# Optimization experiments

Measured on AMD Instinct MI355X. Metric: run time of the kernel, lower is better.

Reference implementation:

```python
import jax, jax.numpy as jnp
import numpy as np

N = 100000      # nodes
E = 1600000     # edges (before self-loops)
IN = 256        # input features
HID = 128       # hidden channels
HEADS = 8
C = HID // HEADS  # per-head channels = 16
L = 3           # num GAT layers
EPS = 1e-5      # batchnorm eps
NEG_SLOPE = 0.2 # leaky relu slope (PyG GATConv default)


def setup_inputs() -> dict:
    key = jax.random.key(0)
    ks = jax.random.split(key, 8)
    s = 0.05
    x = jax.random.normal(ks[0], (N, IN), jnp.float32)
    edge_index = jax.random.randint(ks[1], (2, E), 0, N, dtype=jnp.int32)
    proj_w = jax.random.normal(ks[2], (IN, HID), jnp.float32) * s
    proj_b = jnp.zeros((HID,), jnp.float32)
    W = jax.random.normal(ks[3], (L, HID, HID), jnp.float32) * s
    att_src = jax.random.normal(ks[4], (L, HEADS, C), jnp.float32) * s
    att_dst = jax.random.normal(ks[5], (L, HEADS, C), jnp.float32) * s
    conv_b = jnp.zeros((L, HID), jnp.float32)
    bn_g = jnp.ones((L, HID), jnp.float32)
    bn_b = jnp.zeros((L, HID), jnp.float32)
    fc_w = jax.random.normal(ks[6], (HID, 1), jnp.float32) * s
    fc_b = jnp.zeros((1,), jnp.float32)
    return {"x": x, "edge_index": edge_index, "proj_w": proj_w, "proj_b": proj_b,
            "W": W, "att_src": att_src, "att_dst": att_dst, "conv_b": conv_b,
            "bn_g": bn_g, "bn_b": bn_b, "fc_w": fc_w, "fc_b": fc_b}


def _gat_layer(x, src, dst, W, a_src, a_dst, b):
    # x: [N, HID] -> per-head features h: [N, HEADS, C]
    h = (x @ W).reshape(N, HEADS, C)
    al_src = jnp.einsum('nhc,hc->nh', h, a_src)  # [N, HEADS]
    al_dst = jnp.einsum('nhc,hc->nh', h, a_dst)  # [N, HEADS]
    e = jax.nn.leaky_relu(al_src[src] + al_dst[dst], NEG_SLOPE)  # [Etot, HEADS]
    # segment softmax over edges grouped by destination node
    m = jax.ops.segment_max(e, dst, num_segments=N)              # [N, HEADS]
    w = jnp.exp(e - m[dst])
    denom = jax.ops.segment_sum(w, dst, num_segments=N)          # [N, HEADS]
    alpha = w / (denom[dst] + 1e-16)                             # [Etot, HEADS]
    msg = h[src] * alpha[:, :, None]                             # [Etot, HEADS, C]
    out = jax.ops.segment_sum(msg, dst, num_segments=N)          # [N, HEADS, C]
    return out.reshape(N, HID) + b


def reference(x, edge_index, proj_w, proj_b, W, att_src, att_dst, conv_b, bn_g, bn_b, fc_w, fc_b):
    # add self loops (PyG GATConv default)
    loops = jnp.arange(N, dtype=edge_index.dtype)
    src = jnp.concatenate([edge_index[0], loops])
    dst = jnp.concatenate([edge_index[1], loops])
    h = jax.nn.elu(x @ proj_w + proj_b)
    for i in range(L):
        res = h
        h = _gat_layer(h, src, dst, W[i], att_src[i], att_dst[i], conv_b[i])
        mu = h.mean(axis=0)
        var = h.var(axis=0)  # biased, matches torch BN training math
        h = (h - mu) / jnp.sqrt(var + EPS) * bn_g[i] + bn_b[i]
        h = jax.nn.elu(h)
        h = h + res  # residual; dropout is identity in eval mode
    return h @ fc_w + fc_b
```

## Files before the change

kernel.cpp:

```cpp
#include <hip/hip_runtime.h>
#include <hip/hip_bf16.h>

#define NN 100000
#define EE 1600000
#define ETOT (NN + EE)
#define HID 128
#define HEADS 8
#define CH 16
#define EPS_BN 1e-5f
#define NEG_SLOPE 0.2f
#define NB 196
#define NBLK_A 208

typedef unsigned short ushort_t;
typedef unsigned int uint_t;
typedef __attribute__((ext_vector_type(8))) short short8;
typedef __attribute__((ext_vector_type(4))) float float4v;

__device__ inline uint_t f2bf(float x) {
    __hip_bfloat16 b = __float2bfloat16(x);
    return (uint_t)*reinterpret_cast<unsigned short*>(&b);
}
__device__ inline uint_t pack2(float lo, float hi) {
    return f2bf(lo) | (f2bf(hi) << 16);
}
__device__ inline float bf_lo(uint_t u) { return __uint_as_float(u << 16); }
__device__ inline float bf_hi(uint_t u) { return __uint_as_float(u & 0xffff0000u); }

__global__ __launch_bounds__(256) void bucket_hist(const int* __restrict__ ei,
                                                   int* bcnt, int* lbase) {
    __shared__ int h[256];
    int t = threadIdx.x;
    h[t] = 0;
    __syncthreads();
    int base = blockIdx.x * 8192;
    #pragma unroll 4
    for (int j = 0; j < 32; ++j) {
        int i = base + j * 256 + t;
        if (i < ETOT) {
            int d = (i < EE) ? ei[EE + i] : (i - EE);
            atomicAdd(&h[d >> 9], 1);
        }
    }
    __syncthreads();
    if (t < NB) {
        int v = h[t];
        lbase[blockIdx.x * NB + t] = v ? atomicAdd(&bcnt[t], v) : 0;
    }
}

__global__ void bucket_scan(const int* __restrict__ bcnt, int* bbase, int* rowptr) {
    __shared__ int s[256];
    int t = threadIdx.x;
    int orig = (t < NB) ? bcnt[t] : 0;
    s[t] = orig;
    __syncthreads();
    for (int off = 1; off < 256; off <<= 1) {
        int add = (t >= off) ? s[t - off] : 0;
        __syncthreads();
        s[t] += add;
        __syncthreads();
    }
    if (t < NB) bbase[t] = s[t] - orig;
    if (t == 0) { bbase[NB] = ETOT; rowptr[NN] = ETOT; }
}

__global__ __launch_bounds__(256) void bucket_scatter(const int* __restrict__ ei,
                                                      const int* __restrict__ bbase,
                                                      const int* __restrict__ lbase,
                                                      uint_t* __restrict__ pairs) {
    __shared__ int sbase[256];
    __shared__ int h[256];
    int t = threadIdx.x;
    sbase[t] = (t < NB) ? (bbase[t] + lbase[blockIdx.x * NB + t]) : 0;
    h[t] = 0;
    __syncthreads();
    int base = blockIdx.x * 8192;
    #pragma unroll 4
    for (int j = 0; j < 32; ++j) {
        int i = base + j * 256 + t;
        if (i < ETOT) {
            int sv, dv;
            if (i < EE) { sv = ei[i]; dv = ei[EE + i]; }
            else        { sv = i - EE; dv = sv; }
            int bk = dv >> 9;
            int off = atomicAdd(&h[bk], 1);
            pairs[sbase[bk] + off] = ((uint_t)sv << 9) | (uint_t)(dv & 511);
        }
    }
}

__global__ __launch_bounds__(256) void bucket_build(const uint_t* __restrict__ pairs,
                                                    const int* __restrict__ bbase,
                                                    int* __restrict__ rowptr,
                                                    int* __restrict__ csrc) {
    __shared__ int cnt[512];
    __shared__ int cur[512];
    int b = blockIdx.x;
    int t = threadIdx.x;
    int lo = b << 9;
    int nn = NN - lo; if (nn > 512) nn = 512;
    int e0 = bbase[b];
    int e1 = bbase[b + 1];
    cnt[t] = 0; cnt[t + 256] = 0;
    __syncthreads();
    for (int i = e0 + t; i < e1; i += 256)
        atomicAdd(&cnt[pairs[i] & 511], 1);
    __syncthreads();
    int oc0 = cnt[t], oc1 = cnt[t + 256];
    for (int off = 1; off < 512; off <<= 1) {
        int i0 = t, i1 = t + 256;
        int a0 = cnt[i0] + ((i0 >= off) ? cnt[i0 - off] : 0);
        int a1 = cnt[i1] + ((i1 >= off) ? cnt[i1 - off] : 0);
        __syncthreads();
        cnt[i0] = a0; cnt[i1] = a1;
        __syncthreads();
    }
    int ex0 = cnt[t] - oc0, ex1 = cnt[t + 256] - oc1;
    __syncthreads();
    cur[t] = e0 + ex0; cur[t + 256] = e0 + ex1;
    if (t < nn)       rowptr[lo + t] = e0 + ex0;
    if (t + 256 < nn) rowptr[lo + 256 + t] = e0 + ex1;
    __syncthreads();
    for (int i = e0 + t; i < e1; i += 256) {
        uint_t p = pairs[i];
        int pos = atomicAdd(&cur[p & 511], 1);
        csrc[pos] = (int)(p >> 9);
    }
}


__global__ void castw(const float* __restrict__ proj_w, const float* __restrict__ W,
                      ushort_t* __restrict__ pwT, ushort_t* __restrict__ WT) {
    int id = blockIdx.x * 256 + threadIdx.x;
    if (id < 32768) {
        int n = id >> 8, k = id & 255;
        pwT[id] = (ushort_t)f2bf(proj_w[k * 128 + n]);
    } else if (id < 81920) {
        int id2 = id - 32768;
        int l = id2 >> 14, r = id2 & 16383;
        int n = r >> 7, k = r & 127;
        WT[id2] = (ushort_t)f2bf(W[l * 16384 + k * 128 + n]);
    }
}


__global__ __launch_bounds__(256) void gemm_mfma(
    const void* __restrict__ Aptr, int a_fp32,
    const ushort_t* __restrict__ Bt, int K,
    const float* __restrict__ bias, ushort_t* __restrict__ Cb,
    const float* __restrict__ a_src, const float* __restrict__ a_dst,
    float* __restrict__ al_s, float* __restrict__ al_d, int M)
{
    __shared__ uint4 smem[2304];
    ushort_t* As = (ushort_t*)smem;
    ushort_t* Bs = As + 128 * 72;

    int t = threadIdx.x;
    int row0 = blockIdx.x * 128;
    int lane = t & 63, wv = t >> 6;
    int wm = wv >> 1, wn = wv & 1;
    int lr = lane & 15, quad = lane >> 4;

    float4v acc[4][4] = {};

    for (int k0 = 0; k0 < K; k0 += 64) {
        if (a_fp32) {
            const float* A = (const float*)Aptr;
            #pragma unroll
            for (int j = 0; j < 8; ++j) {
                int idx = j * 256 + t;
                int row = idx >> 4;
                int c4 = (idx & 15) * 4;
                int gr = row0 + row;
                float4 v = make_float4(0.f, 0.f, 0.f, 0.f);
                if (gr < M) v = *(const float4*)(A + (size_t)gr * K + k0 + c4);
                uint2 u; u.x = pack2(v.x, v.y); u.y = pack2(v.z, v.w);
                *(uint2*)&As[row * 72 + c4] = u;
            }
        } else {
            const ushort_t* A = (const ushort_t*)Aptr;
            #pragma unroll
            for (int j = 0; j < 4; ++j) {
                int idx = j * 256 + t;
                int row = idx >> 3;
                int c8 = (idx & 7) * 8;
                int gr = row0 + row;
                uint4 v = make_uint4(0, 0, 0, 0);
                if (gr < M) v = *(const uint4*)(A + (size_t)gr * K + k0 + c8);
                *(uint4*)&As[row * 72 + c8] = v;
            }
        }
        #pragma unroll
        for (int j = 0; j < 4; ++j) {
            int idx = j * 256 + t;
            int row = idx >> 3;
            int c8 = (idx & 7) * 8;
            uint4 v = *(const uint4*)(Bt + (size_t)row * K + k0 + c8);
            *(uint4*)&Bs[row * 72 + c8] = v;
        }
        __syncthreads();

        const ushort_t* Ab = As + (wm * 64 + lr) * 72 + quad * 8;
        const ushort_t* Bb = Bs + (wn * 64 + lr) * 72 + quad * 8;
        #pragma unroll
        for (int ks = 0; ks < 64; ks += 32) {
            short8 a[4], b[4];
            #pragma unroll
            for (int ti = 0; ti < 4; ++ti) a[ti] = *(const short8*)(Ab + ti * 16 * 72 + ks);
            #pragma unroll
            for (int tj = 0; tj < 4; ++tj) b[tj] = *(const short8*)(Bb + tj * 16 * 72 + ks);
            #pragma unroll
            for (int ti = 0; ti < 4; ++ti)
                #pragma unroll
                for (int tj = 0; tj < 4; ++tj)
                    acc[ti][tj] = __builtin_amdgcn_mfma_f32_16x16x32_bf16(
                        a[ti], b[tj], acc[ti][tj], 0, 0, 0);
        }
        __syncthreads();
    }

    float* sc = (float*)smem;
    for (int ti = 0; ti < 4; ++ti) {
        #pragma unroll
        for (int tj = 0; tj < 4; ++tj) {
            #pragma unroll
            for (int r = 0; r < 4; ++r) {
                int rloc = wm * 16 + quad * 4 + r;
                int col = wn * 64 + tj * 16 + lr;
                sc[rloc * 132 + col] = acc[ti][tj][r];
            }
        }
        __syncthreads();
        #pragma unroll
        for (int j = 0; j < 4; ++j) {
            int idx = j * 256 + t;
            int row = idx >> 5;
            int c4 = (idx & 31) * 4;
            float4 v = *(const float4*)&sc[row * 132 + c4];
            int gr = row0 + (row >> 4) * 64 + ti * 16 + (row & 15);
            if (gr < M) {
                if (bias) {
                    float4 bv = *(const float4*)(bias + c4);
                    v.x += bv.x; v.y += bv.y; v.z += bv.z; v.w += bv.w;
                    v.x = v.x > 0.f ? v.x : __expf(v.x) - 1.f;
                    v.y = v.y > 0.f ? v.y : __expf(v.y) - 1.f;
                    v.z = v.z > 0.f ? v.z : __expf(v.z) - 1.f;
                    v.w = v.w > 0.f ? v.w : __expf(v.w) - 1.f;
                }
                uint2 u; u.x = pack2(v.x, v.y); u.y = pack2(v.z, v.w);
                *(uint2*)(Cb + (size_t)gr * 128 + c4) = u;
            }
        }
        if (al_s) {
            int row = t & 31, head = t >> 5;
            int gr = row0 + (row >> 4) * 64 + ti * 16 + (row & 15);
            if (gr < M) {
                const float* rp = &sc[row * 132 + head * 16];
                const float* spv = a_src + head * 16;
                const float* dpv = a_dst + head * 16;
                float s1 = 0.f, s2 = 0.f;
                #pragma unroll
                for (int c = 0; c < 16; ++c) {
                    float hv = rp[c];
                    s1 += hv * spv[c];
                    s2 += hv * dpv[c];
                }
                al_s[gr * 8 + head] = s1;
                al_d[gr * 8 + head] = s2;
            }
        }
        __syncthreads();
    }
}


__global__ __launch_bounds__(256) void gat_agg(
    const int* __restrict__ rowptr, const int* __restrict__ csrc,
    const uint_t* __restrict__ h2b, const float* __restrict__ al_s,
    const float* __restrict__ al_d, const float* __restrict__ bias,
    uint_t* __restrict__ outb)
{
    int wv = (blockIdx.x * blockDim.x + threadIdx.x) >> 6;
    int lane = threadIdx.x & 63;
    if (wv >= NN) return;
    int e0 = rowptr[wv], e1 = rowptr[wv + 1];
    int head = lane >> 3;
    int ch = lane * 2;
    float ald = al_d[wv * HEADS + head];
    float acc0 = 0.f, acc1 = 0.f, denom = 0.f;

    int e = e0;
    for (; e + 8 <= e1; e += 8) {
        int ss[8]; float aa[8]; uint_t pp[8];
        #pragma unroll
        for (int k = 0; k < 8; ++k) ss[k] = csrc[e + k];
        #pragma unroll
        for (int k = 0; k < 8; ++k) aa[k] = al_s[ss[k] * HEADS + head];
        #pragma unroll
        for (int k = 0; k < 8; ++k) pp[k] = h2b[(size_t)ss[k] * 64 + lane];
        #pragma unroll
        for (int k = 0; k < 8; ++k) {
            float x = aa[k] + ald;
            x = fmaxf(x, NEG_SLOPE * x);
            float w = __expf(x);
            acc0 += w * bf_lo(pp[k]);
            acc1 += w * bf_hi(pp[k]);
            denom += w;
        }
    }
    for (; e < e1; ++e) {
        int s = csrc[e];
        float a = al_s[s * HEADS + head];
        uint_t p = h2b[(size_t)s * 64 + lane];
        float x = a + ald;
        x = fmaxf(x, NEG_SLOPE * x);
        float w = __expf(x);
        acc0 += w * bf_lo(p);
        acc1 += w * bf_hi(p);
        denom += w;
    }
    float inv = 1.0f / (denom + 1e-16f);
    outb[(size_t)wv * 64 + lane] = pack2(acc0 * inv + bias[ch], acc1 * inv + bias[ch + 1]);
}


__global__ void bn_stats(const uint_t* __restrict__ ab, float* stats) {
    int t = threadIdx.x;
    int u_idx = t >> 1, hi = t & 1;
    float s = 0.f, q = 0.f;
    for (int r = blockIdx.x; r < NN; r += gridDim.x) {
        uint_t u = ab[(size_t)r * 64 + u_idx];
        float v = hi ? bf_hi(u) : bf_lo(u);
        s += v;
        q += v * v;
    }
    atomicAdd(&stats[t], s);
    atomicAdd(&stats[HID + t], q);
}

__global__ void bn_apply(const uint_t* __restrict__ ab, const float* __restrict__ stats,
                         const float* __restrict__ g, const float* __restrict__ be,
                         uint_t* __restrict__ hb) {
    int i = blockIdx.x * blockDim.x + threadIdx.x;
    if (i >= NN * 32) return;
    int c4 = (i & 31) * 4;
    int nd = i >> 5;
    uint2 av = *(const uint2*)(ab + (size_t)nd * 64 + (c4 >> 1));
    uint2 rv = *(const uint2*)(hb + (size_t)nd * 64 + (c4 >> 1));
    float vv[4] = {bf_lo(av.x), bf_hi(av.x), bf_lo(av.y), bf_hi(av.y)};
    float rr[4] = {bf_lo(rv.x), bf_hi(rv.x), bf_lo(rv.y), bf_hi(rv.y)};
    float o[4];
    #pragma unroll
    for (int j = 0; j < 4; ++j) {
        int c = c4 + j;
        float mu = stats[c] * (1.0f / NN);
        float var = stats[HID + c] * (1.0f / NN) - mu * mu;
        float rs = rsqrtf(var + EPS_BN);
        float x = (vv[j] - mu) * rs * g[c] + be[c];
        x = x > 0.f ? x : __expf(x) - 1.f;
        o[j] = x + rr[j];
    }
    uint2 u; u.x = pack2(o[0], o[1]); u.y = pack2(o[2], o[3]);
    *(uint2*)(hb + (size_t)nd * 64 + (c4 >> 1)) = u;
}


__global__ __launch_bounds__(256) void fc_kernel(
    const uint_t* __restrict__ hb, const float* __restrict__ w,
    const float* __restrict__ b, float* __restrict__ out)
{
    int wv = (blockIdx.x * blockDim.x + threadIdx.x) >> 6;
    int lane = threadIdx.x & 63;
    if (wv >= NN) return;
    uint_t u = hb[(size_t)wv * 64 + lane];
    float2 wl = *(const float2*)(w + lane * 2);
    float acc = bf_lo(u) * wl.x + bf_hi(u) * wl.y;
    #pragma unroll
    for (int off = 32; off > 0; off >>= 1)
        acc += __shfl_down(acc, off, 64);
    if (lane == 0) out[wv] = acc + b[0];
}


extern "C" void kernel_launch(void* const* d_in, const int* in_sizes, int n_in,
                              void* d_out, int out_size, void* d_ws, size_t ws_size,
                              hipStream_t stream) {
    const float* x       = (const float*)d_in[0];
    const int*   ei      = (const int*)  d_in[1];
    const float* proj_w  = (const float*)d_in[2];
    const float* proj_b  = (const float*)d_in[3];
    const float* W       = (const float*)d_in[4];
    const float* att_src = (const float*)d_in[5];
    const float* att_dst = (const float*)d_in[6];
    const float* conv_b  = (const float*)d_in[7];
    const float* bn_g    = (const float*)d_in[8];
    const float* bn_b    = (const float*)d_in[9];
    const float* fc_w    = (const float*)d_in[10];
    const float* fc_b    = (const float*)d_in[11];
    float* out = (float*)d_out;

    char* p = (char*)d_ws;
    uint_t*   hb   = (uint_t*)p;   p += (size_t)NN * 64 * 4;
    uint_t*   h2b  = (uint_t*)p;   p += (size_t)NN * 64 * 4;
    uint_t*   aggb = (uint_t*)p;   p += (size_t)NN * 64 * 4;
    uint_t*   pairs = (uint_t*)aggb;
    float*    al_s = (float*)p;    p += (size_t)NN * HEADS * 4;
    float*    al_d = (float*)p;    p += (size_t)NN * HEADS * 4;
    int* rowptr    = (int*)p;      p += ((size_t)(NN + 1) * 4 + 255) & ~255ull;
    int* csrc      = (int*)p;      p += (size_t)ETOT * 4;
    int* bcnt      = (int*)p;      p += 1024;
    float* stats3  = (float*)p;    p += 3 * 1024;
    int* bbase     = (int*)p;      p += 1024;
    int* lbase     = (int*)p;      p += (size_t)NBLK_A * NB * 4 + 256;
    ushort_t* pwT  = (ushort_t*)p; p += 128 * 256 * 2;
    ushort_t* WT   = (ushort_t*)p; p += 3 * 128 * 128 * 2;
    (void)ws_size; (void)n_in; (void)in_sizes; (void)out_size;

    hipMemsetAsync(bcnt, 0, 4096, stream);

    castw<<<320, 256, 0, stream>>>(proj_w, W, pwT, WT);

    gemm_mfma<<<(NN + 127) / 128, 256, 0, stream>>>(
        x, 1, pwT, 256, proj_b, (ushort_t*)hb, nullptr, nullptr, nullptr, nullptr, NN);

    bucket_hist<<<NBLK_A, 256, 0, stream>>>(ei, bcnt, (int*)lbase);
    bucket_scan<<<1, 256, 0, stream>>>(bcnt, bbase, rowptr);
    bucket_scatter<<<NBLK_A, 256, 0, stream>>>(ei, bbase, (const int*)lbase, pairs);
    bucket_build<<<NB, 256, 0, stream>>>(pairs, bbase, rowptr, csrc);

    for (int l = 0; l < 3; ++l) {
        const ushort_t* WTl = WT + (size_t)l * 128 * 128;
        const float* asl = att_src + (size_t)l * HEADS * CH;
        const float* adl = att_dst + (size_t)l * HEADS * CH;
        const float* cbl = conv_b + (size_t)l * HID;
        const float* gl  = bn_g + (size_t)l * HID;
        const float* bl  = bn_b + (size_t)l * HID;
        float* stl = stats3 + l * 256;

        gemm_mfma<<<(NN + 127) / 128, 256, 0, stream>>>(
            hb, 0, WTl, 128, nullptr, (ushort_t*)h2b, asl, adl, al_s, al_d, NN);
        gat_agg<<<(NN + 3) / 4, 256, 0, stream>>>(rowptr, csrc, h2b, al_s, al_d, cbl, aggb);
        bn_stats<<<512, 128, 0, stream>>>(aggb, stl);
        bn_apply<<<(NN * 32 + 255) / 256, 256, 0, stream>>>(aggb, stl, gl, bl, hb);
    }

    fc_kernel<<<(NN + 3) / 4, 256, 0, stream>>>(hb, fc_w, fc_b, out);
}
```

Before: 845.4 us.

## Fuse BN-apply into next GEMM load and final FC; stage bucket scatter in LDS

The batchnorm-apply/ELU/residual step is folded into the A-tile load of the next layer's GEMM, which also writes the updated residual back to hb. For the last layer it is folded into the final FC reduction, so the standalone bn_apply kernels and their extra passes over the node features go away. Separately, bucket_scatter now runs a local histogram and scan, stages pairs in shared memory sorted by bucket, and writes them out contiguously, replacing scattered global writes with coalesced ones. The cost is about 40KB of extra LDS in the scatter kernel, which may limit occupancy, and more per-element work inside the GEMM load path.

```diff
diff --git a/kernel.cpp b/kernel.cpp
--- a/kernel.cpp
+++ b/kernel.cpp
@@ -69,13 +69,40 @@
                                                       const int* __restrict__ bbase,
                                                       const int* __restrict__ lbase,
                                                       uint_t* __restrict__ pairs) {
+    __shared__ uint_t spair[8192];
+    __shared__ unsigned char sbk[8192];
+    __shared__ int h[256];
+    __shared__ int lscan[256];
     __shared__ int sbase[256];
-    __shared__ int h[256];
-    int t = threadIdx.x;
+    int t = threadIdx.x;
+    int base = blockIdx.x * 8192;
+    int nloc = ETOT - base; if (nloc > 8192) nloc = 8192;
     sbase[t] = (t < NB) ? (bbase[t] + lbase[blockIdx.x * NB + t]) : 0;
     h[t] = 0;
     __syncthreads();
-    int base = blockIdx.x * 8192;
+    #pragma unroll 4
+    for (int j = 0; j < 32; ++j) {
+        int i = base + j * 256 + t;
+        if (i < ETOT) {
+            int d = (i < EE) ? ei[EE + i] : (i - EE);
+            atomicAdd(&h[d >> 9], 1);
+        }
+    }
+    __syncthreads();
+    int orig = h[t];
+    lscan[t] = orig;
+    __syncthreads();
+    for (int off = 1; off < 256; off <<= 1) {
+        int add = (t >= off) ? lscan[t - off] : 0;
+        __syncthreads();
+        lscan[t] += add;
+        __syncthreads();
+    }
+    int excl = lscan[t] - orig;
+    __syncthreads();
+    lscan[t] = excl;
+    h[t] = excl;
+    __syncthreads();
     #pragma unroll 4
     for (int j = 0; j < 32; ++j) {
         int i = base + j * 256 + t;
@@ -84,8 +111,18 @@
             if (i < EE) { sv = ei[i]; dv = ei[EE + i]; }
             else        { sv = i - EE; dv = sv; }
             int bk = dv >> 9;
-            int off = atomicAdd(&h[bk], 1);
-            pairs[sbase[bk] + off] = ((uint_t)sv << 9) | (uint_t)(dv & 511);
+            int lp = atomicAdd(&h[bk], 1);
+            spair[lp] = ((uint_t)sv << 9) | (uint_t)(dv & 511);
+            sbk[lp] = (unsigned char)bk;
+        }
+    }
+    __syncthreads();
+    #pragma unroll 4
+    for (int j = 0; j < 32; ++j) {
+        int i = j * 256 + t;
+        if (i < nloc) {
+            int bk = sbk[i];
+            pairs[sbase[bk] + (i - lscan[bk])] = spair[i];
         }
     }
 }
@@ -146,13 +183,16 @@
 
 
 __global__ __launch_bounds__(256) void gemm_mfma(
-    const void* __restrict__ Aptr, int a_fp32,
+    const void* __restrict__ Aptr, int mode,
     const ushort_t* __restrict__ Bt, int K,
     const float* __restrict__ bias, ushort_t* __restrict__ Cb,
     const float* __restrict__ a_src, const float* __restrict__ a_dst,
-    float* __restrict__ al_s, float* __restrict__ al_d, int M)
+    float* __restrict__ al_s, float* __restrict__ al_d, int M,
+    uint_t* __restrict__ hbio, const float* __restrict__ stats,
+    const float* __restrict__ bn_gl, const float* __restrict__ bn_bl)
 {
     __shared__ uint4 smem[2304];
+    __shared__ float2 scsh[128];
     ushort_t* As = (ushort_t*)smem;
     ushort_t* Bs = As + 128 * 72;
 
@@ -162,10 +202,18 @@
     int wm = wv >> 1, wn = wv & 1;
     int lr = lane & 15, quad = lane >> 4;
 
+    if (mode == 2 && t < 128) {
+        float mu = stats[t] * (1.0f / NN);
+        float var = stats[128 + t] * (1.0f / NN) - mu * mu;
+        float s = bn_gl[t] * rsqrtf(var + EPS_BN);
+        scsh[t] = make_float2(s, bn_bl[t] - mu * s);
+    }
+    __syncthreads();
+
     float4v acc[4][4] = {};
 
     for (int k0 = 0; k0 < K; k0 += 64) {
-        if (a_fp32) {
+        if (mode == 1) {
             const float* A = (const float*)Aptr;
             #pragma unroll
             for (int j = 0; j < 8; ++j) {
@@ -178,7 +226,7 @@
                 uint2 u; u.x = pack2(v.x, v.y); u.y = pack2(v.z, v.w);
                 *(uint2*)&As[row * 72 + c4] = u;
             }
-        } else {
+        } else if (mode == 0) {
             const ushort_t* A = (const ushort_t*)Aptr;
             #pragma unroll
             for (int j = 0; j < 4; ++j) {
@@ -189,6 +237,41 @@
                 uint4 v = make_uint4(0, 0, 0, 0);
                 if (gr < M) v = *(const uint4*)(A + (size_t)gr * K + k0 + c8);
                 *(uint4*)&As[row * 72 + c8] = v;
+            }
+        } else {
+            const uint_t* agg = (const uint_t*)Aptr;
+            #pragma unroll
+            for (int j = 0; j < 4; ++j) {
+                int idx = j * 256 + t;
+                int row = idx >> 3;
+                int u4 = idx & 7;
+                int gr = row0 + row;
+                uint4 o = make_uint4(0, 0, 0, 0);
+                if (gr < M) {
+                    size_t gi = (size_t)gr * 64 + (k0 >> 1) + u4 * 4;
+                    uint4 av = *(const uint4*)(agg + gi);
+                    uint4 rv = *(const uint4*)(hbio + gi);
+                    int cb = k0 + u4 * 8;
+                    uint_t aa[4] = {av.x, av.y, av.z, av.w};
+                    uint_t rr[4] = {rv.x, rv.y, rv.z, rv.w};
+                    float ov[8];
+                    #pragma unroll
+                    for (int q = 0; q < 4; ++q) {
+                        float2 s0 = scsh[cb + 2 * q];
+                        float2 s1 = scsh[cb + 2 * q + 1];
+                        float x0 = s0.x * bf_lo(aa[q]) + s0.y;
+                        x0 = x0 > 0.f ? x0 : __expf(x0) - 1.f;
+                        x0 += bf_lo(rr[q]);
+                        float x1 = s1.x * bf_hi(aa[q]) + s1.y;
+                        x1 = x1 > 0.f ? x1 : __expf(x1) - 1.f;
+                        x1 += bf_hi(rr[q]);
+                        ov[2 * q] = x0; ov[2 * q + 1] = x1;
+                    }
+                    o.x = pack2(ov[0], ov[1]); o.y = pack2(ov[2], ov[3]);
+                    o.z = pack2(ov[4], ov[5]); o.w = pack2(ov[6], ov[7]);
+                    *(uint4*)(hbio + gi) = o;
+                }
+                *(uint4*)&As[row * 72 + u4 * 8] = o;
             }
         }
         #pragma unroll
@@ -339,47 +422,41 @@
     atomicAdd(&stats[HID + t], q);
 }
 
-__global__ void bn_apply(const uint_t* __restrict__ ab, const float* __restrict__ stats,
-                         const float* __restrict__ g, const float* __restrict__ be,
-                         uint_t* __restrict__ hb) {
-    int i = blockIdx.x * blockDim.x + threadIdx.x;
-    if (i >= NN * 32) return;
-    int c4 = (i & 31) * 4;
-    int nd = i >> 5;
-    uint2 av = *(const uint2*)(ab + (size_t)nd * 64 + (c4 >> 1));
-    uint2 rv = *(const uint2*)(hb + (size_t)nd * 64 + (c4 >> 1));
-    float vv[4] = {bf_lo(av.x), bf_hi(av.x), bf_lo(av.y), bf_hi(av.y)};
-    float rr[4] = {bf_lo(rv.x), bf_hi(rv.x), bf_lo(rv.y), bf_hi(rv.y)};
-    float o[4];
-    #pragma unroll
-    for (int j = 0; j < 4; ++j) {
-        int c = c4 + j;
-        float mu = stats[c] * (1.0f / NN);
-        float var = stats[HID + c] * (1.0f / NN) - mu * mu;
-        float rs = rsqrtf(var + EPS_BN);
-        float x = (vv[j] - mu) * rs * g[c] + be[c];
-        x = x > 0.f ? x : __expf(x) - 1.f;
-        o[j] = x + rr[j];
-    }
-    uint2 u; u.x = pack2(o[0], o[1]); u.y = pack2(o[2], o[3]);
-    *(uint2*)(hb + (size_t)nd * 64 + (c4 >> 1)) = u;
-}
-
-
-__global__ __launch_bounds__(256) void fc_kernel(
-    const uint_t* __restrict__ hb, const float* __restrict__ w,
-    const float* __restrict__ b, float* __restrict__ out)
+
+__global__ __launch_bounds__(256) void fc_fused(
+    const uint_t* __restrict__ aggb, const uint_t* __restrict__ hb,
+    const float* __restrict__ stats, const float* __restrict__ g,
+    const float* __restrict__ be, const float* __restrict__ w,
+    const float* __restrict__ fb, float* __restrict__ out)
 {
-    int wv = (blockIdx.x * blockDim.x + threadIdx.x) >> 6;
-    int lane = threadIdx.x & 63;
+    __shared__ float2 scsh[128];
+    int t = threadIdx.x;
+    if (t < 128) {
+        float mu = stats[t] * (1.0f / NN);
+        float var = stats[128 + t] * (1.0f / NN) - mu * mu;
+        float s = g[t] * rsqrtf(var + EPS_BN);
+        scsh[t] = make_float2(s, be[t] - mu * s);
+    }
+    __syncthreads();
+    int wv = (blockIdx.x * 256 + t) >> 6;
+    int lane = t & 63;
     if (wv >= NN) return;
-    uint_t u = hb[(size_t)wv * 64 + lane];
-    float2 wl = *(const float2*)(w + lane * 2);
-    float acc = bf_lo(u) * wl.x + bf_hi(u) * wl.y;
+    uint_t av = aggb[(size_t)wv * 64 + lane];
+    uint_t rv = hb[(size_t)wv * 64 + lane];
+    int c = lane * 2;
+    float2 s0 = scsh[c], s1 = scsh[c + 1];
+    float x0 = s0.x * bf_lo(av) + s0.y;
+    x0 = x0 > 0.f ? x0 : __expf(x0) - 1.f;
+    x0 += bf_lo(rv);
+    float x1 = s1.x * bf_hi(av) + s1.y;
+    x1 = x1 > 0.f ? x1 : __expf(x1) - 1.f;
+    x1 += bf_hi(rv);
+    float2 wl = *(const float2*)(w + c);
+    float acc = x0 * wl.x + x1 * wl.y;
     #pragma unroll
     for (int off = 32; off > 0; off >>= 1)
         acc += __shfl_down(acc, off, 64);
-    if (lane == 0) out[wv] = acc + b[0];
+    if (lane == 0) out[wv] = acc + fb[0];
 }
 
 
@@ -422,7 +499,8 @@
     castw<<<320, 256, 0, stream>>>(proj_w, W, pwT, WT);
 
     gemm_mfma<<<(NN + 127) / 128, 256, 0, stream>>>(
-        x, 1, pwT, 256, proj_b, (ushort_t*)hb, nullptr, nullptr, nullptr, nullptr, NN);
+        x, 1, pwT, 256, proj_b, (ushort_t*)hb, nullptr, nullptr, nullptr, nullptr, NN,
+        nullptr, nullptr, nullptr, nullptr);
 
     bucket_hist<<<NBLK_A, 256, 0, stream>>>(ei, bcnt, (int*)lbase);
     bucket_scan<<<1, 256, 0, stream>>>(bcnt, bbase, rowptr);
@@ -434,16 +512,22 @@
         const float* asl = att_src + (size_t)l * HEADS * CH;
         const float* adl = att_dst + (size_t)l * HEADS * CH;
         const float* cbl = conv_b + (size_t)l * HID;
-        const float* gl  = bn_g + (size_t)l * HID;
-        const float* bl  = bn_b + (size_t)l * HID;
         float* stl = stats3 + l * 256;
 
-        gemm_mfma<<<(NN + 127) / 128, 256, 0, stream>>>(
-            hb, 0, WTl, 128, nullptr, (ushort_t*)h2b, asl, adl, al_s, al_d, NN);
+        if (l == 0) {
+            gemm_mfma<<<(NN + 127) / 128, 256, 0, stream>>>(
+                hb, 0, WTl, 128, nullptr, (ushort_t*)h2b, asl, adl, al_s, al_d, NN,
+                nullptr, nullptr, nullptr, nullptr);
+        } else {
+            gemm_mfma<<<(NN + 127) / 128, 256, 0, stream>>>(
+                aggb, 2, WTl, 128, nullptr, (ushort_t*)h2b, asl, adl, al_s, al_d, NN,
+                hb, stats3 + (l - 1) * 256, bn_g + (size_t)(l - 1) * HID,
+                bn_b + (size_t)(l - 1) * HID);
+        }
         gat_agg<<<(NN + 3) / 4, 256, 0, stream>>>(rowptr, csrc, h2b, al_s, al_d, cbl, aggb);
         bn_stats<<<512, 128, 0, stream>>>(aggb, stl);
-        bn_apply<<<(NN * 32 + 255) / 256, 256, 0, stream>>>(aggb, stl, gl, bl, hb);
-    }
-
-    fc_kernel<<<(NN + 3) / 4, 256, 0, stream>>>(hb, fc_w, fc_b, out);
-}
+    }
+
+    fc_fused<<<(NN + 3) / 4, 256, 0, stream>>>(
+        aggb, hb, stats3 + 2 * 256, bn_g + 2 * HID, bn_b + 2 * HID, fc_w, fc_b, out);
+}
```

Result: no change. 836.7 us (-1.0%).
